# Kernel optimization log

Measured on AMD Instinct MI355X. Metric: run time of the kernel, lower is better.

## Reference

```python
import jax, jax.numpy as jnp
import numpy as np

K = 16          # per-chain hidden states: int(sqrt(args.hidden_dim=256))
K2 = K * K      # joint enumerated state (w, x)
SCALE = 1.0     # handlers.scale(scale=args.scale)


def setup_inputs() -> dict:
    key = jax.random.key(0)
    ks = jax.random.split(key, 8)
    N, T, D, B = 4096, 512, 88, 1024
    # Bernoulli observations (binary piano-roll style data)
    sequences = (jax.random.uniform(ks[0], (N, T, D)) < 0.3).astype(jnp.float32)
    lengths = jax.random.randint(ks[1], (N,), T // 4, T + 1).astype(jnp.int32)
    mb = jax.random.randint(ks[2], (B,), 0, N).astype(jnp.int32)
    mask = jnp.ones((B,), dtype=bool)

    def simplex(k, shape):
        p = jax.random.uniform(k, shape) + 0.1
        return p / p.sum(-1, keepdims=True)

    probs_w = simplex(ks[3], (K, K))
    probs_x = simplex(ks[4], (K, K))
    w_init = simplex(ks[5], (K,))
    x_init = simplex(ks[6], (K,))
    probs_y = jax.random.uniform(ks[7], (K, K, D), minval=0.05, maxval=0.95)
    return dict(sequences=sequences, probs_w=probs_w, probs_x=probs_x,
                w_init=w_init, x_init=x_init, probs_y=probs_y,
                lengths=lengths, mb=mb, mask=mask)


def reference(sequences, probs_w, probs_x, w_init, x_init, probs_y, lengths, mb, mask):
    """Exact marginal log-likelihood of the factorial HMM (what parallel
    enumeration over w_t, x_t computes): forward algorithm over the joint
    256-state chain with factorized transitions and Bernoulli emissions."""
    T = sequences.shape[1]
    seq = sequences[mb]          # [B, T, D]
    len_mb = lengths[mb]         # [B]

    # Bernoulli emission log-probs, contracted over tones plate (dim -1):
    # logB[t, b, k] = sum_d [ y*log(p) + (1-y)*log(1-p) ],  k = (w, x) flat
    logp = jnp.log(probs_y).reshape(K2, -1)       # [K2, D]
    log1mp = jnp.log1p(-probs_y).reshape(K2, -1)  # [K2, D]
    logB = jnp.einsum('btd,kd->tbk', seq, logp - log1mp) + log1mp.sum(-1)  # [T,B,K2]

    # Factorized joint transition: logT[(w,x),(w',x')] = log p(w'|w) + log p(x'|x)
    logT = (jnp.log(probs_w)[:, None, :, None] +
            jnp.log(probs_x)[None, :, None, :]).reshape(K2, K2)
    log_init = (jnp.log(w_init)[:, None] + jnp.log(x_init)[None, :]).reshape(K2)

    alpha0 = log_init + logB[0]  # [B, K2]; all lengths >= 1 here

    def step(alpha, inp):
        logb_t, t = inp
        nxt = jax.nn.logsumexp(alpha[:, :, None] + logT[None], axis=1) + logb_t
        valid = (t < len_mb)[:, None]            # mask: t < lengths[mb]
        return jnp.where(valid, nxt, alpha), None

    alpha, _ = jax.lax.scan(step, alpha0, (logB[1:], jnp.arange(1, T)))
    loglik = jax.nn.logsumexp(alpha, axis=-1)    # [B]
    return SCALE * jnp.sum(jnp.where(mask, loglik, 0.0))
```

## Files before the change

kernel.cpp:

```cpp
#include <hip/hip_runtime.h>


typedef _Float16 h4 __attribute__((ext_vector_type(4)));
typedef _Float16 h8 __attribute__((ext_vector_type(8)));
typedef float v4f __attribute__((ext_vector_type(4)));

#define TT 512
#define DD 88
#define NB 1024
#define LOG4096 8.317766167f

#define WS_E    0ull
#define WS_M    268435456ull
#define WS_BF   (WS_M + 2097152ull)
#define WS_BIAS (WS_BF + 49152ull)
#define WS_WF   (WS_BIAS + 1024ull)
#define WS_XF   (WS_WF + 512ull)

__global__ __launch_bounds__(256) void prep_kernel(
    const float* __restrict__ pw, const float* __restrict__ px,
    const float* __restrict__ py, float* __restrict__ out,
    unsigned char* __restrict__ ws) {
  int tid = threadIdx.x;
  int blk = blockIdx.x;
  _Float16* bfrag = (_Float16*)(ws + WS_BF);
  float* bias = (float*)(ws + WS_BIAS);
  _Float16* wf = (_Float16*)(ws + WS_WF);
  _Float16* xf = (_Float16*)(ws + WS_XF);
  if (blk == 0) {
    float s = 0.f;
    for (int d = 0; d < DD; ++d) s += __logf(1.0f - py[tid * DD + d]);
    bias[tid] = s;
  } else if (blk == 1) {
    if (tid == 0) out[0] = 0.0f;
    if (tid < 64) {
      int q = tid >> 4, c = tid & 15;
      #pragma unroll
      for (int i = 0; i < 4; ++i) {
        wf[tid * 4 + i] = (_Float16)pw[(4 * q + i) * 16 + c];
        xf[tid * 4 + i] = (_Float16)px[(4 * q + i) * 16 + c];
      }
    }
  } else {
    int idx = (blk - 2) * 256 + tid;
    int j = idx & 7, l = (idx >> 3) & 63, n = (idx >> 9) & 15, c = idx >> 13;
    int state = n * 16 + (l & 15);
    int d = c * 32 + (l >> 4) * 8 + j;
    float v = 0.f;
    if (d < DD) {
      float p = py[state * DD + d];
      v = __logf(p) - __logf(1.0f - p);
    }
    bfrag[idx] = (_Float16)v;
  }
}

__global__ __launch_bounds__(256) void emis_kernel(
    const float* __restrict__ seq, const int* __restrict__ lengths,
    const int* __restrict__ mb, unsigned char* __restrict__ ws) {
  int b = blockIdx.x >> 3;
  int blk8 = blockIdx.x & 7;
  int item = mb[b];
  int len = lengths[item];
  if (blk8 * 64 >= len) return;
  __shared__ uint4 lbf[3072];
  int tid = threadIdx.x;
  const uint4* gbf = (const uint4*)(ws + WS_BF);
  #pragma unroll
  for (int i = 0; i < 12; ++i) lbf[tid + 256 * i] = gbf[tid + 256 * i];
  __syncthreads();
  int wave = tid >> 6, lane = tid & 63;
  int t0 = (blk8 * 4 + wave) * 16;
  if (t0 >= len) return;
  int q = lane >> 4, cc = lane & 15;
  const float* srow = seq + ((size_t)item * TT + (t0 + cc)) * DD;
  h8 af[3];
  #pragma unroll
  for (int c = 0; c < 3; ++c) {
    int d0 = c * 32 + q * 8;
    h8 a;
    if (d0 < DD) {
      float4 f0 = *(const float4*)(srow + d0);
      float4 f1 = *(const float4*)(srow + d0 + 4);
      a[0] = (_Float16)f0.x; a[1] = (_Float16)f0.y;
      a[2] = (_Float16)f0.z; a[3] = (_Float16)f0.w;
      a[4] = (_Float16)f1.x; a[5] = (_Float16)f1.y;
      a[6] = (_Float16)f1.z; a[7] = (_Float16)f1.w;
    } else {
      #pragma unroll
      for (int j = 0; j < 8; ++j) a[j] = (_Float16)0.f;
    }
    af[c] = a;
  }
  v4f acc[16];
  #pragma unroll
  for (int n = 0; n < 16; ++n) acc[n] = (v4f){0.f, 0.f, 0.f, 0.f};
  #pragma unroll
  for (int n = 0; n < 16; ++n) {
    #pragma unroll
    for (int c = 0; c < 3; ++c) {
      union { uint4 u; h8 h; } bf;
      bf.u = lbf[(c * 16 + n) * 64 + lane];
      acc[n] = __builtin_amdgcn_mfma_f32_16x16x32_f16(af[c], bf.h, acc[n], 0, 0, 0);
    }
  }
  const float* bias = (const float*)(ws + WS_BIAS);
  #pragma unroll
  for (int n = 0; n < 16; ++n) {
    float bn = bias[16 * n + cc];
    acc[n][0] += bn; acc[n][1] += bn; acc[n][2] += bn; acc[n][3] += bn;
  }
  float mrow[4];
  #pragma unroll
  for (int r = 0; r < 4; ++r) {
    float mv = acc[0][r];
    #pragma unroll
    for (int n = 1; n < 16; ++n) mv = fmaxf(mv, acc[n][r]);
    mv = fmaxf(mv, __shfl_xor(mv, 1));
    mv = fmaxf(mv, __shfl_xor(mv, 2));
    mv = fmaxf(mv, __shfl_xor(mv, 4));
    mv = fmaxf(mv, __shfl_xor(mv, 8));
    mrow[r] = mv;
  }
  float* marr = (float*)(ws + WS_M);
  if (cc == 0) {
    float4 mm;
    mm.x = mrow[0]; mm.y = mrow[1]; mm.z = mrow[2]; mm.w = mrow[3];
    *(float4*)(marr + b * TT + t0 + 4 * q) = mm;
  }
  _Float16* E = (_Float16*)(ws + WS_E);
  #pragma unroll
  for (int r = 0; r < 4; ++r) {
    int tt = t0 + 4 * q + r;
    union { _Float16 h[16]; uint4 u[2]; } pk;
    #pragma unroll
    for (int n = 0; n < 16; ++n)
      pk.h[n] = (_Float16)__expf(acc[n][r] - mrow[r]);
    uint4* dst = (uint4*)(E + ((size_t)b * TT + tt) * 256 + cc * 16);
    dst[0] = pk.u[0];
    dst[1] = pk.u[1];
  }
}

#define LOADCH(EA, MA, tbase)                                          \
  {                                                                    \
    _Pragma("unroll") for (int i2 = 0; i2 < 8; ++i2) {                 \
      int tt = (tbase) + i2;                                           \
      tt = tt < (TT - 1) ? tt : (TT - 1);                              \
      EA[i2] = *(const uint2*)(Eb + ((size_t)tt << 8) + off);          \
      MA[i2] = M[tt];                                                  \
    }                                                                  \
  }

#define STEPCH(EA, MA)                                                 \
  {                                                                    \
    _Pragma("unroll") for (int i2 = 0; i2 < 8; ++i2) {                 \
      if (t >= len) { done = true; break; }                            \
      float Rn = s0 + s1 + s2 + s3;                                    \
      Rn += __shfl_xor(Rn, 1); Rn += __shfl_xor(Rn, 2);                \
      Rn += __shfl_xor(Rn, 4); Rn += __shfl_xor(Rn, 8);                \
      Rn += __shfl_xor(Rn, 16); Rn += __shfl_xor(Rn, 32);              \
      h4 a1;                                                           \
      a1[0] = (_Float16)s0; a1[1] = (_Float16)s1;                      \
      a1[2] = (_Float16)s2; a1[3] = (_Float16)s3;                      \
      v4f zz = (v4f){0.f, 0.f, 0.f, 0.f};                              \
      v4f d1 = __builtin_amdgcn_mfma_f32_16x16x16f16(a1, Wf, zz, 0, 0, 0); \
      h4 a2;                                                           \
      a2[0] = (_Float16)d1[0]; a2[1] = (_Float16)d1[1];                \
      a2[2] = (_Float16)d1[2]; a2[3] = (_Float16)d1[3];                \
      v4f d2 = __builtin_amdgcn_mfma_f32_16x16x16f16(a2, Xf, zz, 0, 0, 0); \
      union { uint2 u; h4 h; } bt;                                     \
      bt.u = EA[i2];                                                   \
      float f = __builtin_amdgcn_rcpf(Rn) * 4096.0f;                   \
      s0 = d2[0] * (float)bt.h[0] * f;                                 \
      s1 = d2[1] * (float)bt.h[1] * f;                                 \
      s2 = d2[2] * (float)bt.h[2] * f;                                 \
      s3 = d2[3] * (float)bt.h[3] * f;                                 \
      logacc += __logf(Rn) + MA[i2] - LOG4096;                         \
      ++t;                                                             \
    }                                                                  \
  }

__global__ __launch_bounds__(64) void fwd_kernel(
    const int* __restrict__ lengths, const int* __restrict__ mb,
    const float* __restrict__ w_init, const float* __restrict__ x_init,
    float* __restrict__ out, const unsigned char* __restrict__ ws) {
  int b = blockIdx.x;
  int lane = threadIdx.x;
  int q = lane >> 4, cc = lane & 15;
  int item = mb[b];
  int len = lengths[item];
  const _Float16* Eb = (const _Float16*)(ws + WS_E) + (size_t)b * (TT * 256);
  const float* M = (const float*)(ws + WS_M) + b * TT;
  union { uint2 u; h4 h; } wfu, xfu;
  wfu.u = *(const uint2*)((const _Float16*)(ws + WS_WF) + lane * 4);
  xfu.u = *(const uint2*)((const _Float16*)(ws + WS_XF) + lane * 4);
  h4 Wf = wfu.h, Xf = xfu.h;
  int off = cc * 16 + 4 * q;
  union { uint2 u; h4 h; } bt0;
  bt0.u = *(const uint2*)(Eb + off);
  float xiv = x_init[cc] * 4096.0f;
  float s0 = w_init[4 * q + 0] * xiv * (float)bt0.h[0];
  float s1 = w_init[4 * q + 1] * xiv * (float)bt0.h[1];
  float s2 = w_init[4 * q + 2] * xiv * (float)bt0.h[2];
  float s3 = w_init[4 * q + 3] * xiv * (float)bt0.h[3];
  float logacc = M[0] - LOG4096;
  uint2 eA[8], eB[8];
  float mA[8], mB[8];
  LOADCH(eA, mA, 1);
  LOADCH(eB, mB, 9);
  int t = 1;
  int nextbase = 17;
  bool done = (len <= 1);
  while (!done) {
    STEPCH(eA, mA);
    if (done) break;
    LOADCH(eA, mA, nextbase);
    nextbase += 8;
    STEPCH(eB, mB);
    if (done) break;
    LOADCH(eB, mB, nextbase);
    nextbase += 8;
  }
  float Sf = s0 + s1 + s2 + s3;
  Sf += __shfl_xor(Sf, 1); Sf += __shfl_xor(Sf, 2); Sf += __shfl_xor(Sf, 4);
  Sf += __shfl_xor(Sf, 8); Sf += __shfl_xor(Sf, 16); Sf += __shfl_xor(Sf, 32);
  float ll = logacc + __logf(Sf);
  if (lane == 0) atomicAdd(out, ll);
}

extern "C" void kernel_launch(void* const* d_in, const int* in_sizes, int n_in,
                              void* d_out, int out_size, void* d_ws, size_t ws_size,
                              hipStream_t stream) {
  const float* seq = (const float*)d_in[0];
  const float* pw = (const float*)d_in[1];
  const float* px = (const float*)d_in[2];
  const float* wi = (const float*)d_in[3];
  const float* xi = (const float*)d_in[4];
  const float* py = (const float*)d_in[5];
  const int* lengths = (const int*)d_in[6];
  const int* mb = (const int*)d_in[7];
  float* out = (float*)d_out;
  unsigned char* ws = (unsigned char*)d_ws;

  prep_kernel<<<98, 256, 0, stream>>>(pw, px, py, out, ws);
  emis_kernel<<<NB * 8, 256, 0, stream>>>(seq, lengths, mb, ws);
  fwd_kernel<<<NB, 64, 0, stream>>>(lengths, mb, wi, xi, out, ws);
}
```

Measured before the change: 1.022 ms.

## Use DPP wave reduction, fp16 forward state, larger prefetch, LDS bias

Replaces the six-step shfl_xor wave sum in the serial forward recurrence with a DPP row-shift/broadcast reduction plus readlane. The state is now kept as packed fp16 and multiplied in fp16, so the per-step float-to-half conversions disappear. Emission prefetch chunks grow from 8 to 16 steps, and the emission kernel stages its bias in LDS. The goal is a shorter per-step dependency chain in the latency-bound recurrence. In exchange, fp16 state products carry less precision and more registers are used.

New measurement: 1.022 ms. About the same (-0.1%).

```diff
diff --git a/kernel.cpp b/kernel.cpp
--- a/kernel.cpp
+++ b/kernel.cpp
@@ -16,6 +16,23 @@
 #define WS_BIAS (WS_BF + 49152ull)
 #define WS_WF   (WS_BIAS + 1024ull)
 #define WS_XF   (WS_WF + 512ull)
+
+__device__ inline float dpp_wave_sum(float x) {
+  union fi { float f; int i; };
+  fi v; v.f = x;
+#define DPPADD(ctrl, rmask)                                              \
+  { fi t; t.i = __builtin_amdgcn_update_dpp(0, v.i, ctrl, rmask, 0xf, false); \
+    v.f += t.f; }
+  DPPADD(0x111, 0xf)
+  DPPADD(0x112, 0xf)
+  DPPADD(0x114, 0xf)
+  DPPADD(0x118, 0xf)
+  DPPADD(0x142, 0xa)
+  DPPADD(0x143, 0xc)
+#undef DPPADD
+  fi o; o.i = __builtin_amdgcn_readlane(v.i, 63);
+  return o.f;
+}
 
 __global__ __launch_bounds__(256) void prep_kernel(
     const float* __restrict__ pw, const float* __restrict__ px,
@@ -64,10 +81,12 @@
   int len = lengths[item];
   if (blk8 * 64 >= len) return;
   __shared__ uint4 lbf[3072];
+  __shared__ float lbias[256];
   int tid = threadIdx.x;
   const uint4* gbf = (const uint4*)(ws + WS_BF);
   #pragma unroll
   for (int i = 0; i < 12; ++i) lbf[tid + 256 * i] = gbf[tid + 256 * i];
+  lbias[tid] = ((const float*)(ws + WS_BIAS))[tid];
   __syncthreads();
   int wave = tid >> 6, lane = tid & 63;
   int t0 = (blk8 * 4 + wave) * 16;
@@ -104,10 +123,9 @@
       acc[n] = __builtin_amdgcn_mfma_f32_16x16x32_f16(af[c], bf.h, acc[n], 0, 0, 0);
     }
   }
-  const float* bias = (const float*)(ws + WS_BIAS);
   #pragma unroll
   for (int n = 0; n < 16; ++n) {
-    float bn = bias[16 * n + cc];
+    float bn = lbias[16 * n + cc];
     acc[n][0] += bn; acc[n][1] += bn; acc[n][2] += bn; acc[n][3] += bn;
   }
   float mrow[4];
@@ -144,7 +162,7 @@
 
 #define LOADCH(EA, MA, tbase)                                          \
   {                                                                    \
-    _Pragma("unroll") for (int i2 = 0; i2 < 8; ++i2) {                 \
+    _Pragma("unroll") for (int i2 = 0; i2 < 16; ++i2) {                \
       int tt = (tbase) + i2;                                           \
       tt = tt < (TT - 1) ? tt : (TT - 1);                              \
       EA[i2] = *(const uint2*)(Eb + ((size_t)tt << 8) + off);          \
@@ -154,28 +172,29 @@
 
 #define STEPCH(EA, MA)                                                 \
   {                                                                    \
-    _Pragma("unroll") for (int i2 = 0; i2 < 8; ++i2) {                 \
+    _Pragma("unroll") for (int i2 = 0; i2 < 16; ++i2) {                \
       if (t >= len) { done = true; break; }                            \
-      float Rn = s0 + s1 + s2 + s3;                                    \
-      Rn += __shfl_xor(Rn, 1); Rn += __shfl_xor(Rn, 2);                \
-      Rn += __shfl_xor(Rn, 4); Rn += __shfl_xor(Rn, 8);                \
-      Rn += __shfl_xor(Rn, 16); Rn += __shfl_xor(Rn, 32);              \
-      h4 a1;                                                           \
-      a1[0] = (_Float16)s0; a1[1] = (_Float16)s1;                      \
-      a1[2] = (_Float16)s2; a1[3] = (_Float16)s3;                      \
+      float rl = (float)sv[0] + (float)sv[1] +                         \
+                 (float)sv[2] + (float)sv[3];                          \
+      float Rn = dpp_wave_sum(rl);                                     \
       v4f zz = (v4f){0.f, 0.f, 0.f, 0.f};                              \
-      v4f d1 = __builtin_amdgcn_mfma_f32_16x16x16f16(a1, Wf, zz, 0, 0, 0); \
+      v4f d1 = __builtin_amdgcn_mfma_f32_16x16x16f16(sv, Wf, zz, 0, 0, 0); \
       h4 a2;                                                           \
-      a2[0] = (_Float16)d1[0]; a2[1] = (_Float16)d1[1];                \
-      a2[2] = (_Float16)d1[2]; a2[3] = (_Float16)d1[3];                \
+      { auto lo = __builtin_amdgcn_cvt_pkrtz(d1[0], d1[1]);            \
+        auto hi = __builtin_amdgcn_cvt_pkrtz(d1[2], d1[3]);            \
+        a2[0] = lo[0]; a2[1] = lo[1]; a2[2] = hi[0]; a2[3] = hi[1]; }  \
       v4f d2 = __builtin_amdgcn_mfma_f32_16x16x16f16(a2, Xf, zz, 0, 0, 0); \
       union { uint2 u; h4 h; } bt;                                     \
       bt.u = EA[i2];                                                   \
-      float f = __builtin_amdgcn_rcpf(Rn) * 4096.0f;                   \
-      s0 = d2[0] * (float)bt.h[0] * f;                                 \
-      s1 = d2[1] * (float)bt.h[1] * f;                                 \
-      s2 = d2[2] * (float)bt.h[2] * f;                                 \
-      s3 = d2[3] * (float)bt.h[3] * f;                                 \
+      h4 pm;                                                           \
+      { auto lo = __builtin_amdgcn_cvt_pkrtz(d2[0], d2[1]);            \
+        auto hi = __builtin_amdgcn_cvt_pkrtz(d2[2], d2[3]);            \
+        pm[0] = lo[0]; pm[1] = lo[1]; pm[2] = hi[0]; pm[3] = hi[1]; }  \
+      pm = pm * bt.h;                                                  \
+      float fsc = __builtin_amdgcn_rcpf(Rn) * 4096.0f;                 \
+      _Float16 fh = (_Float16)fsc;                                     \
+      h4 fv; fv[0] = fh; fv[1] = fh; fv[2] = fh; fv[3] = fh;           \
+      sv = pm * fv;                                                    \
       logacc += __logf(Rn) + MA[i2] - LOG4096;                         \
       ++t;                                                             \
     }                                                                  \
@@ -200,31 +219,31 @@
   union { uint2 u; h4 h; } bt0;
   bt0.u = *(const uint2*)(Eb + off);
   float xiv = x_init[cc] * 4096.0f;
-  float s0 = w_init[4 * q + 0] * xiv * (float)bt0.h[0];
-  float s1 = w_init[4 * q + 1] * xiv * (float)bt0.h[1];
-  float s2 = w_init[4 * q + 2] * xiv * (float)bt0.h[2];
-  float s3 = w_init[4 * q + 3] * xiv * (float)bt0.h[3];
+  h4 sv;
+  sv[0] = (_Float16)(w_init[4 * q + 0] * xiv * (float)bt0.h[0]);
+  sv[1] = (_Float16)(w_init[4 * q + 1] * xiv * (float)bt0.h[1]);
+  sv[2] = (_Float16)(w_init[4 * q + 2] * xiv * (float)bt0.h[2]);
+  sv[3] = (_Float16)(w_init[4 * q + 3] * xiv * (float)bt0.h[3]);
   float logacc = M[0] - LOG4096;
-  uint2 eA[8], eB[8];
-  float mA[8], mB[8];
+  uint2 eA[16], eB[16];
+  float mA[16], mB[16];
   LOADCH(eA, mA, 1);
-  LOADCH(eB, mB, 9);
+  LOADCH(eB, mB, 17);
   int t = 1;
-  int nextbase = 17;
+  int nextbase = 33;
   bool done = (len <= 1);
   while (!done) {
     STEPCH(eA, mA);
     if (done) break;
     LOADCH(eA, mA, nextbase);
-    nextbase += 8;
+    nextbase += 16;
     STEPCH(eB, mB);
     if (done) break;
     LOADCH(eB, mB, nextbase);
-    nextbase += 8;
-  }
-  float Sf = s0 + s1 + s2 + s3;
-  Sf += __shfl_xor(Sf, 1); Sf += __shfl_xor(Sf, 2); Sf += __shfl_xor(Sf, 4);
-  Sf += __shfl_xor(Sf, 8); Sf += __shfl_xor(Sf, 16); Sf += __shfl_xor(Sf, 32);
+    nextbase += 16;
+  }
+  float Sf = dpp_wave_sum((float)sv[0] + (float)sv[1] +
+                          (float)sv[2] + (float)sv[3]);
   float ll = logacc + __logf(Sf);
   if (lane == 0) atomicAdd(out, ll);
 }
```
